# Kernel optimization log

Measured on AMD Instinct MI355X. Metric: run time of the kernel, lower is better.

## Reference

```python
import jax, jax.numpy as jnp
import numpy as np

B, L, IN_LEN = 1, 1024, 512
D_MODEL, N_LAYERS = 1024, 4
D_INNER = 2 * D_MODEL
D_STATE = 16
DT_RANK = D_MODEL // 16  # 64
D_CONV = 4
EPS = 1e-5


def setup_inputs() -> dict:
    key = jax.random.key(0)
    ks = jax.random.split(key, 12)
    s = 0.02
    # dt bias init as in mamba_ssm: softplus^{-1}(dt) with dt ~ logUniform(1e-3, 1e-1)
    dt = jnp.exp(jax.random.uniform(ks[7], (N_LAYERS, D_INNER)) * (jnp.log(0.1) - jnp.log(0.001)) + jnp.log(0.001))
    dt_bias = dt + jnp.log(-jnp.expm1(-dt))
    A_log = jnp.log(jnp.broadcast_to(jnp.arange(1, D_STATE + 1, dtype=jnp.float32), (N_LAYERS, D_INNER, D_STATE)))
    return {
        "input": jax.random.normal(ks[0], (B, L, IN_LEN), jnp.float32),
        "inference_parameters": 0,
        "input_w": jax.random.normal(ks[1], (D_MODEL, IN_LEN), jnp.float32) * s,
        "norm_w": jnp.ones((N_LAYERS, D_MODEL), jnp.float32),
        "norm_b": jnp.zeros((N_LAYERS, D_MODEL), jnp.float32),
        "in_proj_w": jax.random.normal(ks[2], (N_LAYERS, 2 * D_INNER, D_MODEL), jnp.float32) * s,
        "conv_w": jax.random.normal(ks[3], (N_LAYERS, D_INNER, D_CONV), jnp.float32) * 0.3,
        "conv_b": jnp.zeros((N_LAYERS, D_INNER), jnp.float32),
        "x_proj_w": jax.random.normal(ks[4], (N_LAYERS, DT_RANK + 2 * D_STATE, D_INNER), jnp.float32) * s,
        "dt_proj_w": jax.random.normal(ks[5], (N_LAYERS, D_INNER, DT_RANK), jnp.float32) * (DT_RANK ** -0.5),
        "dt_proj_b": dt_bias,
        "A_log": A_log,
        "ssm_D": jnp.ones((N_LAYERS, D_INNER), jnp.float32),
        "out_proj_w": jax.random.normal(ks[6], (N_LAYERS, D_MODEL, D_INNER), jnp.float32) * s,
    }


def _layer_norm(x, w, b):
    mu = x.mean(-1, keepdims=True)
    xc = x - mu
    var = (xc * xc).mean(-1, keepdims=True)
    return xc * jax.lax.rsqrt(var + EPS) * w + b


def _mamba(h, ipw, cw, cb, xpw, dtw, dtb, a_log, d_skip, opw):
    # h: [B, L, D_MODEL]
    seqlen = h.shape[1]
    xz = jnp.einsum('bld,ed->ble', h, ipw)  # [B, L, 2*D_INNER]
    x, z = jnp.split(xz, 2, axis=-1)
    # causal depthwise conv1d (kernel D_CONV, left pad D_CONV-1)
    xp = jnp.pad(x, ((0, 0), (D_CONV - 1, 0), (0, 0)))
    x = sum(cw[:, k] * xp[:, k:k + seqlen, :] for k in range(D_CONV)) + cb
    x = jax.nn.silu(x)
    x_dbl = jnp.einsum('bld,ed->ble', x, xpw)  # [B, L, DT_RANK + 2*D_STATE]
    dt = x_dbl[..., :DT_RANK]
    Bc = x_dbl[..., DT_RANK:DT_RANK + D_STATE]  # [B, L, D_STATE]
    Cc = x_dbl[..., DT_RANK + D_STATE:]          # [B, L, D_STATE]
    delta = jax.nn.softplus(jnp.einsum('blr,dr->bld', dt, dtw) + dtb)  # [B, L, D_INNER]
    A = -jnp.exp(a_log)                          # [D_INNER, D_STATE]
    dA = jnp.exp(delta[..., None] * A)           # [B, L, D_INNER, D_STATE]
    dBu = delta[..., None] * Bc[:, :, None, :] * x[..., None]

    def step(hc, t):
        dA_t, dBu_t, C_t = t
        hc = dA_t * hc + dBu_t                   # [B, D_INNER, D_STATE]
        return hc, jnp.einsum('bds,bs->bd', hc, C_t)

    h0 = jnp.zeros((x.shape[0], D_INNER, D_STATE), x.dtype)
    _, ys = jax.lax.scan(step, h0, (dA.transpose(1, 0, 2, 3), dBu.transpose(1, 0, 2, 3), Cc.transpose(1, 0, 2)))
    y = ys.transpose(1, 0, 2) + x * d_skip       # [B, L, D_INNER]
    y = y * jax.nn.silu(z)
    return jnp.einsum('bld,ed->ble', y, opw)     # [B, L, D_MODEL]


def reference(input, inference_parameters, input_w, norm_w, norm_b, in_proj_w, conv_w, conv_b, x_proj_w, dt_proj_w, dt_proj_b, A_log, ssm_D, out_proj_w):
    h = jnp.einsum('bli,di->bld', input, input_w)  # input_layer (no bias)
    res = None
    for i in range(N_LAYERS):
        res = h if res is None else h + res
        hn = _layer_norm(res, norm_w[i], norm_b[i])
        h = _mamba(hn, in_proj_w[i], conv_w[i], conv_b[i], x_proj_w[i], dt_proj_w[i], dt_proj_b[i], A_log[i], ssm_D[i], out_proj_w[i])
    # NOTE: the source forward returns hidden_states directly (norm_f is never applied)
    return h
```

## Files before the change

kernel.cpp:

```cpp
#include <hip/hip_runtime.h>
#include <hip/hip_bf16.h>
#include <math.h>

#define L_SEQ   1024
#define DMODEL  1024
#define DINNER  2048
#define DSTATE  16
#define DTRANK  64
#define NXP     96
#define LN_EPS  1e-5f
#define CHUNK   32
#define NCHUNK  (L_SEQ / CHUNK)
#define SK(l)   ((l) + ((l) >> 5))

typedef __bf16 bf16x8 __attribute__((ext_vector_type(8)));
typedef float  f32x4  __attribute__((ext_vector_type(4)));

__global__ __launch_bounds__(256)
void gemm_bt_bf16(const __hip_bfloat16* __restrict__ A,
                  const __hip_bfloat16* __restrict__ W,
                  float* __restrict__ C,
                  int K, int lda, int ldb, int ldc) {
    __shared__ __hip_bfloat16 As[128][32];
    __shared__ __hip_bfloat16 Bs[128][32];
    const int tid  = threadIdx.x;
    const int lane = tid & 63;
    const int wave = tid >> 6;
    const int m0 = blockIdx.y * 128, n0 = blockIdx.x * 128;
    const int wm = (wave >> 1) * 64, wn = (wave & 1) * 64;
    const int srow = tid >> 2, skcol = (tid & 3) << 3;
    const int fm = lane & 15, fk = (lane >> 4) << 3;

    f32x4 acc[4][4] = {};

    const __hip_bfloat16* Ap0 = A + (size_t)(m0 + srow) * lda + skcol;
    const __hip_bfloat16* Ap1 = Ap0 + (size_t)64 * lda;
    const __hip_bfloat16* Wp0 = W + (size_t)(n0 + srow) * ldb + skcol;
    const __hip_bfloat16* Wp1 = Wp0 + (size_t)64 * ldb;

    for (int k0 = 0; k0 < K; k0 += 32) {
        __syncthreads();
        __builtin_amdgcn_global_load_lds(
            (const __attribute__((address_space(1))) unsigned int*)(Ap0 + k0),
            (__attribute__((address_space(3))) unsigned int*)&As[srow][skcol], 16, 0, 0);
        __builtin_amdgcn_global_load_lds(
            (const __attribute__((address_space(1))) unsigned int*)(Ap1 + k0),
            (__attribute__((address_space(3))) unsigned int*)&As[64 + srow][skcol], 16, 0, 0);
        __builtin_amdgcn_global_load_lds(
            (const __attribute__((address_space(1))) unsigned int*)(Wp0 + k0),
            (__attribute__((address_space(3))) unsigned int*)&Bs[srow][skcol], 16, 0, 0);
        __builtin_amdgcn_global_load_lds(
            (const __attribute__((address_space(1))) unsigned int*)(Wp1 + k0),
            (__attribute__((address_space(3))) unsigned int*)&Bs[64 + srow][skcol], 16, 0, 0);
        __syncthreads();

        bf16x8 af[4], bfr[4];
        #pragma unroll
        for (int i = 0; i < 4; ++i) {
            af[i]  = *(const bf16x8*)&As[wm + i * 16 + fm][fk];
            bfr[i] = *(const bf16x8*)&Bs[wn + i * 16 + fm][fk];
        }
        #pragma unroll
        for (int mt = 0; mt < 4; ++mt)
            #pragma unroll
            for (int nt = 0; nt < 4; ++nt)
                acc[mt][nt] = __builtin_amdgcn_mfma_f32_16x16x32_bf16(
                    af[mt], bfr[nt], acc[mt][nt], 0, 0, 0);
    }

    const int crow = (lane >> 4) << 2;
    const int ccol = lane & 15;
    #pragma unroll
    for (int mt = 0; mt < 4; ++mt)
        #pragma unroll
        for (int nt = 0; nt < 4; ++nt) {
            float* cp = C + (size_t)(m0 + wm + mt * 16 + crow) * ldc
                          + n0 + wn + nt * 16 + ccol;
            #pragma unroll
            for (int r = 0; r < 4; ++r) cp[(size_t)r * ldc] = acc[mt][nt][r];
        }
}

__global__ __launch_bounds__(256)
void gemm_nt(const float* __restrict__ A, const float* __restrict__ W,
             float* __restrict__ C, int M, int N, int K,
             int lda, int ldb, int ldc) {
    __shared__ float As[16][64];
    __shared__ float Bs[16][64];
    const int tid = threadIdx.x;
    const int tx = tid & 15, ty = tid >> 4;
    const int m0 = blockIdx.y * 64, n0 = blockIdx.x * 64;
    const int lr = tid >> 2;
    const int lk = (tid & 3) << 2;
    float acc[4][4] = {};

    for (int k0 = 0; k0 < K; k0 += 16) {
        float4 av = make_float4(0.f, 0.f, 0.f, 0.f);
        float4 bv = make_float4(0.f, 0.f, 0.f, 0.f);
        const int am = m0 + lr;
        if (am < M) av = *(const float4*)(A + (size_t)am * lda + k0 + lk);
        const int bn = n0 + lr;
        if (bn < N) bv = *(const float4*)(W + (size_t)bn * ldb + k0 + lk);
        __syncthreads();
        As[lk + 0][lr] = av.x; As[lk + 1][lr] = av.y;
        As[lk + 2][lr] = av.z; As[lk + 3][lr] = av.w;
        Bs[lk + 0][lr] = bv.x; Bs[lk + 1][lr] = bv.y;
        Bs[lk + 2][lr] = bv.z; Bs[lk + 3][lr] = bv.w;
        __syncthreads();
        #pragma unroll
        for (int k = 0; k < 16; ++k) {
            const float4 a = *(const float4*)&As[k][ty << 2];
            const float4 b = *(const float4*)&Bs[k][tx << 2];
            acc[0][0] += a.x * b.x; acc[0][1] += a.x * b.y;
            acc[0][2] += a.x * b.z; acc[0][3] += a.x * b.w;
            acc[1][0] += a.y * b.x; acc[1][1] += a.y * b.y;
            acc[1][2] += a.y * b.z; acc[1][3] += a.y * b.w;
            acc[2][0] += a.z * b.x; acc[2][1] += a.z * b.y;
            acc[2][2] += a.z * b.z; acc[2][3] += a.z * b.w;
            acc[3][0] += a.w * b.x; acc[3][1] += a.w * b.y;
            acc[3][2] += a.w * b.z; acc[3][3] += a.w * b.w;
        }
    }
    #pragma unroll
    for (int i = 0; i < 4; ++i) {
        const int m = m0 + (ty << 2) + i;
        if (m < M) {
            #pragma unroll
            for (int j = 0; j < 4; ++j) {
                const int n = n0 + (tx << 2) + j;
                if (n < N) C[(size_t)m * ldc + n] = acc[i][j];
            }
        }
    }
}

__global__ __launch_bounds__(256)
void gemm_nn_softplus(const float* __restrict__ A, const float* __restrict__ B,
                      const float* __restrict__ bias, float* __restrict__ C,
                      int K, int lda, int ldb, int ldc) {
    __shared__ float As[16][64];
    __shared__ float Bs[16][64];
    const int t = threadIdx.x;
    const int tx = t & 15, ty = t >> 4;
    const int m0 = blockIdx.y * 64, n0 = blockIdx.x * 64;
    const int ar = t >> 2, ak = (t & 3) << 2;
    const int bk = t >> 4, bn = (t & 15) << 2;
    float acc[4][4] = {};

    for (int k0 = 0; k0 < K; k0 += 16) {
        const float4 av = *(const float4*)(A + (size_t)(m0 + ar) * lda + k0 + ak);
        const float4 bv = *(const float4*)(B + (size_t)(k0 + bk) * ldb + n0 + bn);
        __syncthreads();
        As[ak + 0][ar] = av.x; As[ak + 1][ar] = av.y;
        As[ak + 2][ar] = av.z; As[ak + 3][ar] = av.w;
        *(float4*)&Bs[bk][bn] = bv;
        __syncthreads();
        #pragma unroll
        for (int k = 0; k < 16; ++k) {
            const float4 a = *(const float4*)&As[k][ty << 2];
            const float4 b = *(const float4*)&Bs[k][tx << 2];
            acc[0][0] += a.x * b.x; acc[0][1] += a.x * b.y;
            acc[0][2] += a.x * b.z; acc[0][3] += a.x * b.w;
            acc[1][0] += a.y * b.x; acc[1][1] += a.y * b.y;
            acc[1][2] += a.y * b.z; acc[1][3] += a.y * b.w;
            acc[2][0] += a.z * b.x; acc[2][1] += a.z * b.y;
            acc[2][2] += a.z * b.z; acc[2][3] += a.z * b.w;
            acc[3][0] += a.w * b.x; acc[3][1] += a.w * b.y;
            acc[3][2] += a.w * b.z; acc[3][3] += a.w * b.w;
        }
    }
    #pragma unroll
    for (int i = 0; i < 4; ++i) {
        const int m = m0 + (ty << 2) + i;
        const float bb = bias[m];
        #pragma unroll
        for (int j = 0; j < 4; ++j) {
            const int n = n0 + (tx << 2) + j;
            const float v = acc[i][j] + bb;
            C[(size_t)m * ldc + n] = (v > 20.f) ? v : log1pf(expf(v));
        }
    }
}

__global__ __launch_bounds__(256)
void gemm_nn_splitk(const float* __restrict__ A, const float* __restrict__ B,
                    float* __restrict__ C, int lda, int ldb, int ldc, int kchunk) {
    __shared__ float As[32][32];
    __shared__ float Bs[32][64];
    const int t = threadIdx.x;
    const int tx = t & 15, ty = t >> 4;
    const int m0 = blockIdx.y * 32, n0 = blockIdx.x * 64;
    const int k0s = blockIdx.z * kchunk;
    const int ar = t >> 3, ak = (t & 7) << 2;
    const int bk = t >> 4, bn = (t & 15) << 2;
    float acc[2][4] = {};

    for (int k0 = k0s; k0 < k0s + kchunk; k0 += 32) {
        const float4 av = *(const float4*)(A + (size_t)(m0 + ar) * lda + k0 + ak);
        const float4 bv0 = *(const float4*)(B + (size_t)(k0 + bk) * ldb + n0 + bn);
        const float4 bv1 = *(const float4*)(B + (size_t)(k0 + bk + 16) * ldb + n0 + bn);
        __syncthreads();
        As[ak + 0][ar] = av.x; As[ak + 1][ar] = av.y;
        As[ak + 2][ar] = av.z; As[ak + 3][ar] = av.w;
        *(float4*)&Bs[bk][bn] = bv0;
        *(float4*)&Bs[bk + 16][bn] = bv1;
        __syncthreads();
        #pragma unroll
        for (int k = 0; k < 32; ++k) {
            const float a0 = As[k][(ty << 1) + 0];
            const float a1 = As[k][(ty << 1) + 1];
            const float4 b = *(const float4*)&Bs[k][tx << 2];
            acc[0][0] += a0 * b.x; acc[0][1] += a0 * b.y;
            acc[0][2] += a0 * b.z; acc[0][3] += a0 * b.w;
            acc[1][0] += a1 * b.x; acc[1][1] += a1 * b.y;
            acc[1][2] += a1 * b.z; acc[1][3] += a1 * b.w;
        }
    }
    #pragma unroll
    for (int i = 0; i < 2; ++i) {
        const int m = m0 + (ty << 1) + i;
        #pragma unroll
        for (int j = 0; j < 4; ++j)
            atomicAdd(&C[(size_t)m * ldc + n0 + (tx << 2) + j], acc[i][j]);
    }
}

__global__ __launch_bounds__(256)
void zero_f32(float* __restrict__ p, int n) {
    const int i = blockIdx.x * 256 + threadIdx.x;
    if (i < n) p[i] = 0.f;
}

__global__ __launch_bounds__(256)
void cast_f32_bf16(const float* __restrict__ in, __hip_bfloat16* __restrict__ out,
                   int n4) {
    const int i = blockIdx.x * 256 + threadIdx.x;
    if (i < n4) {
        const float4 v = *(const float4*)(in + (size_t)i * 4);
        __hip_bfloat16 h0 = __float2bfloat16(v.x), h1 = __float2bfloat16(v.y);
        __hip_bfloat16 h2 = __float2bfloat16(v.z), h3 = __float2bfloat16(v.w);
        ushort4 p;
        p.x = *(unsigned short*)&h0; p.y = *(unsigned short*)&h1;
        p.z = *(unsigned short*)&h2; p.w = *(unsigned short*)&h3;
        *(ushort4*)((unsigned short*)out + (size_t)i * 4) = p;
    }
}

__global__ __launch_bounds__(256)
void transpose_bc(const float* __restrict__ xdbl_T, float* __restrict__ xbc) {
    __shared__ float tile[32][33];
    const int t = threadIdx.x;
    const int l0 = blockIdx.x * 32;
    const int s = t >> 3, lc = (t & 7) << 2;
    const float4 v = *(const float4*)(xdbl_T + (size_t)(DTRANK + s) * L_SEQ + l0 + lc);
    tile[s][lc + 0] = v.x; tile[s][lc + 1] = v.y;
    tile[s][lc + 2] = v.z; tile[s][lc + 3] = v.w;
    __syncthreads();
    const int l = t >> 3, sc = (t & 7) << 2;
    float4 w;
    w.x = tile[sc + 0][l]; w.y = tile[sc + 1][l];
    w.z = tile[sc + 2][l]; w.w = tile[sc + 3][l];
    *(float4*)(xbc + (size_t)(l0 + l) * 32 + sc) = w;
}

__global__ __launch_bounds__(256)
void transpose_bf16(const unsigned short* __restrict__ in,
                    unsigned short* __restrict__ out, int R, int Cc) {
    __shared__ unsigned short tile[64][65];
    const int t = threadIdx.x;
    const int r0 = blockIdx.y * 64, c0 = blockIdx.x * 64;
    const int tr = t >> 3, tc8 = (t & 7) << 3;
    #pragma unroll
    for (int i = 0; i < 2; ++i) {
        const int r = tr + i * 32;
        const ushort4 v0 = *(const ushort4*)(in + (size_t)(r0 + r) * Cc + c0 + tc8);
        const ushort4 v1 = *(const ushort4*)(in + (size_t)(r0 + r) * Cc + c0 + tc8 + 4);
        tile[r][tc8 + 0] = v0.x; tile[r][tc8 + 1] = v0.y;
        tile[r][tc8 + 2] = v0.z; tile[r][tc8 + 3] = v0.w;
        tile[r][tc8 + 4] = v1.x; tile[r][tc8 + 5] = v1.y;
        tile[r][tc8 + 6] = v1.z; tile[r][tc8 + 7] = v1.w;
    }
    __syncthreads();
    #pragma unroll
    for (int i = 0; i < 2; ++i) {
        const int r = tr + i * 32;
        ushort4 w0, w1;
        w0.x = tile[tc8 + 0][r]; w0.y = tile[tc8 + 1][r];
        w0.z = tile[tc8 + 2][r]; w0.w = tile[tc8 + 3][r];
        w1.x = tile[tc8 + 4][r]; w1.y = tile[tc8 + 5][r];
        w1.z = tile[tc8 + 6][r]; w1.w = tile[tc8 + 7][r];
        *(ushort4*)(out + (size_t)(c0 + r) * R + r0 + tc8)     = w0;
        *(ushort4*)(out + (size_t)(c0 + r) * R + r0 + tc8 + 4) = w1;
    }
}

__global__ __launch_bounds__(256)
void add_ln(const float* __restrict__ h, float* __restrict__ res,
            __hip_bfloat16* __restrict__ hn, const float* __restrict__ w,
            const float* __restrict__ b, int is_first) {
    const int l = blockIdx.x;
    const int t = threadIdx.x;
    float v[4];
    float s = 0.f, ss = 0.f;
    #pragma unroll
    for (int j = 0; j < 4; ++j) {
        const int d = t + j * 256;
        float x = h[(size_t)l * DMODEL + d];
        if (!is_first) x += res[(size_t)l * DMODEL + d];
        res[(size_t)l * DMODEL + d] = x;
        v[j] = x; s += x; ss += x * x;
    }
    #pragma unroll
    for (int o = 32; o > 0; o >>= 1) {
        s  += __shfl_down(s, o);
        ss += __shfl_down(ss, o);
    }
    __shared__ float sm[4], sm2[4];
    const int wid = t >> 6;
    if ((t & 63) == 0) { sm[wid] = s; sm2[wid] = ss; }
    __syncthreads();
    s  = sm[0] + sm[1] + sm[2] + sm[3];
    ss = sm2[0] + sm2[1] + sm2[2] + sm2[3];
    const float mu  = s * (1.f / DMODEL);
    const float var = ss * (1.f / DMODEL) - mu * mu;
    const float r   = rsqrtf(var + LN_EPS);
    #pragma unroll
    for (int j = 0; j < 4; ++j) {
        const int d = t + j * 256;
        hn[(size_t)l * DMODEL + d] = __float2bfloat16((v[j] - mu) * r * w[d] + b[d]);
    }
}

__global__ __launch_bounds__(256)
void conv_silu_t(const float* __restrict__ xz_T, float* __restrict__ xc_T,
                 const float* __restrict__ cw, const float* __restrict__ cb) {
    const int d = blockIdx.x;
    const int t = threadIdx.x;
    __shared__ float row[L_SEQ];
    *(float4*)&row[t << 2] = *(const float4*)(xz_T + (size_t)d * L_SEQ + (t << 2));
    __syncthreads();
    const float w0 = cw[d * 4 + 0], w1 = cw[d * 4 + 1];
    const float w2 = cw[d * 4 + 2], w3 = cw[d * 4 + 3];
    const float bb = cb[d];
    float o[4];
    #pragma unroll
    for (int j = 0; j < 4; ++j) {
        const int l = (t << 2) + j;
        float acc = bb + w3 * row[l];
        if (l >= 1) acc += w2 * row[l - 1];
        if (l >= 2) acc += w1 * row[l - 2];
        if (l >= 3) acc += w0 * row[l - 3];
        const float sig = 1.f / (1.f + __expf(-acc));
        o[j] = acc * sig;
    }
    *(float4*)(xc_T + (size_t)d * L_SEQ + (t << 2)) = make_float4(o[0], o[1], o[2], o[3]);
}

__global__ __launch_bounds__(512)
void ssm_scan_t(const float* __restrict__ delta_T,
                const float* __restrict__ xc_T,
                const float* __restrict__ xbc,
                const float* __restrict__ xz_T,
                const float* __restrict__ alog,
                const float* __restrict__ dsk,
                __hip_bfloat16* __restrict__ y_T) {
    const int d = blockIdx.x;
    const int t = threadIdx.x;
    const int s = t & 15;
    const int c = t >> 4;

    __shared__ float sdl[L_SEQ + 32], sxl[L_SEQ + 32];
    __shared__ float sz[L_SEQ], sy[L_SEQ];
    __shared__ float saprod[NCHUNK][DSTATE];
    __shared__ float shloc[NCHUNK][DSTATE];
    __shared__ float shstart[NCHUNK][DSTATE];

    if (t < 256) {
        const float4 v = ((const float4*)(delta_T + (size_t)d * L_SEQ))[t];
        const int l = t << 2;
        sdl[SK(l)] = v.x; sdl[SK(l + 1)] = v.y;
        sdl[SK(l + 2)] = v.z; sdl[SK(l + 3)] = v.w;
        ((float4*)sz)[t] = ((const float4*)(xz_T + (size_t)(DINNER + d) * L_SEQ))[t];
    } else {
        const int tt = t - 256;
        const float4 v = ((const float4*)(xc_T + (size_t)d * L_SEQ))[tt];
        const int l = tt << 2;
        sxl[SK(l)] = v.x; sxl[SK(l + 1)] = v.y;
        sxl[SK(l + 2)] = v.z; sxl[SK(l + 3)] = v.w;
    }
    __syncthreads();

    const float A  = -expf(alog[d * DSTATE + s]);
    const int   l0 = c * CHUNK;

    float aprod = 1.f, h = 0.f;
    #pragma unroll 4
    for (int j = 0; j < CHUNK; ++j) {
        const int l = l0 + j;
        const float dl = sdl[SK(l)];
        const float da = __expf(dl * A);
        h = da * h + dl * xbc[(size_t)l * 32 + s] * sxl[SK(l)];
        aprod *= da;
    }
    saprod[c][s] = aprod;
    shloc[c][s]  = h;
    __syncthreads();

    if (c == 0) {
        float hs = 0.f;
        for (int cc = 0; cc < NCHUNK; ++cc) {
            shstart[cc][s] = hs;
            hs = saprod[cc][s] * hs + shloc[cc][s];
        }
    }
    __syncthreads();

    h = shstart[c][s];
    const float Dk = dsk[d];
    #pragma unroll 4
    for (int j = 0; j < CHUNK; ++j) {
        const int l = l0 + j;
        const float dl = sdl[SK(l)];
        const float xl = sxl[SK(l)];
        h = __expf(dl * A) * h + dl * xbc[(size_t)l * 32 + s] * xl;
        float cch = h * xbc[(size_t)l * 32 + 16 + s];
        cch += __shfl_xor(cch, 1, 16);
        cch += __shfl_xor(cch, 2, 16);
        cch += __shfl_xor(cch, 4, 16);
        cch += __shfl_xor(cch, 8, 16);
        if (s == 0) {
            const float zl  = sz[l];
            const float sig = 1.f / (1.f + __expf(-zl));
            sy[l] = (cch + xl * Dk) * (zl * sig);
        }
    }
    __syncthreads();

    if (t < 256) {
        const float4 v = ((const float4*)sy)[t];
        __hip_bfloat16 h0 = __float2bfloat16(v.x), h1 = __float2bfloat16(v.y);
        __hip_bfloat16 h2 = __float2bfloat16(v.z), h3 = __float2bfloat16(v.w);
        ushort4 p;
        p.x = *(unsigned short*)&h0; p.y = *(unsigned short*)&h1;
        p.z = *(unsigned short*)&h2; p.w = *(unsigned short*)&h3;
        *(ushort4*)((unsigned short*)y_T + (size_t)d * L_SEQ + (t << 2)) = p;
    }
}

extern "C" void kernel_launch(void* const* d_in, const int* in_sizes, int n_in,
                              void* d_out, int out_size, void* d_ws, size_t ws_size,
                              hipStream_t stream) {
    const float* input   = (const float*)d_in[0];
    const float* input_w = (const float*)d_in[2];
    const float* norm_w  = (const float*)d_in[3];
    const float* norm_b  = (const float*)d_in[4];
    const float* ipw     = (const float*)d_in[5];
    const float* cw      = (const float*)d_in[6];
    const float* cb      = (const float*)d_in[7];
    const float* xpw     = (const float*)d_in[8];
    const float* dtw     = (const float*)d_in[9];
    const float* dtb     = (const float*)d_in[10];
    const float* alog    = (const float*)d_in[11];
    const float* dsk     = (const float*)d_in[12];
    const float* opw     = (const float*)d_in[13];
    float* out = (float*)d_out;

    float* ws      = (float*)d_ws;
    float* h       = ws;
    float* res     = h       + (1u << 20);
    float* xz_T    = res     + (1u << 20);
    float* xc_T    = xz_T    + (4u << 20);
    float* xdbl_T  = xc_T    + (2u << 20);
    float* xbc     = xdbl_T  + (NXP * L_SEQ);
    float* delta_T = xbc     + (L_SEQ * 32);
    __hip_bfloat16* hn_bf  = (__hip_bfloat16*)(delta_T + (2u << 20));
    __hip_bfloat16* yT_bf  = hn_bf  + (1u << 20);
    __hip_bfloat16* y_bf   = yT_bf  + (2u << 20);
    __hip_bfloat16* ipw_bf = y_bf   + (2u << 20);
    __hip_bfloat16* opw_bf = ipw_bf + (4u << 20);

    const dim3 blk(256);

    gemm_nt<<<dim3(DMODEL / 64, L_SEQ / 64), blk, 0, stream>>>(
        input, input_w, h, L_SEQ, DMODEL, 512, 512, 512, DMODEL);

    for (int i = 0; i < 4; ++i) {
        cast_f32_bf16<<<(2 * DINNER * DMODEL / 4 + 255) / 256, blk, 0, stream>>>(
            ipw + (size_t)i * 2 * DINNER * DMODEL, ipw_bf, 2 * DINNER * DMODEL / 4);

        add_ln<<<L_SEQ, 256, 0, stream>>>(
            h, res, hn_bf, norm_w + i * DMODEL, norm_b + i * DMODEL, i == 0);

        gemm_bt_bf16<<<dim3(L_SEQ / 128, 2 * DINNER / 128), blk, 0, stream>>>(
            ipw_bf, hn_bf, xz_T, DMODEL, DMODEL, DMODEL, L_SEQ);

        conv_silu_t<<<DINNER, 256, 0, stream>>>(
            xz_T, xc_T, cw + i * DINNER * 4, cb + i * DINNER);

        zero_f32<<<(NXP * L_SEQ + 255) / 256, blk, 0, stream>>>(xdbl_T, NXP * L_SEQ);
        gemm_nn_splitk<<<dim3(L_SEQ / 64, 3, 8), blk, 0, stream>>>(
            xpw + (size_t)i * NXP * DINNER, xc_T, xdbl_T,
            DINNER, L_SEQ, L_SEQ, DINNER / 8);

        transpose_bc<<<L_SEQ / 32, 256, 0, stream>>>(xdbl_T, xbc);

        gemm_nn_softplus<<<dim3(L_SEQ / 64, DINNER / 64), blk, 0, stream>>>(
            dtw + (size_t)i * DINNER * DTRANK, xdbl_T, dtb + i * DINNER, delta_T,
            DTRANK, DTRANK, L_SEQ, L_SEQ);

        ssm_scan_t<<<DINNER, 512, 0, stream>>>(
            delta_T, xc_T, xbc, xz_T,
            alog + i * DINNER * DSTATE, dsk + i * DINNER, yT_bf);

        transpose_bf16<<<dim3(L_SEQ / 64, DINNER / 64), blk, 0, stream>>>(
            (const unsigned short*)yT_bf, (unsigned short*)y_bf, DINNER, L_SEQ);

        cast_f32_bf16<<<(DMODEL * DINNER / 4 + 255) / 256, blk, 0, stream>>>(
            opw + (size_t)i * DMODEL * DINNER, opw_bf, DMODEL * DINNER / 4);
        float* dst = (i == 3) ? out : h;
        gemm_bt_bf16<<<dim3(DMODEL / 128, L_SEQ / 128), blk, 0, stream>>>(
            y_bf, opw_bf, dst, DINNER, DINNER, DINNER, DMODEL);
    }
}
```

Measured before the change: 906.1 us.

## Halve scan chunk size, reuse chunk-local states, and split-K the out_proj GEMM

The SSM scan now uses 1024 threads with 16-step chunks. Each thread keeps its per-step cumulative decay and local state in registers, so the second pass becomes one fused multiply-add per step instead of recomputing the exponential recurrence. The out_proj GEMM, which launched only 64 blocks, is split four ways along K with atomicAdd into a zeroed output to fill more compute units. The costs are extra register pressure, a longer serial inter-chunk pass (64 chunks), an extra zeroing kernel, and atomic traffic with non-deterministic summation order.

```diff
diff --git a/kernel.cpp b/kernel.cpp
--- a/kernel.cpp
+++ b/kernel.cpp
@@ -9,7 +9,7 @@
 #define DTRANK  64
 #define NXP     96
 #define LN_EPS  1e-5f
-#define CHUNK   32
+#define CHUNK   16
 #define NCHUNK  (L_SEQ / CHUNK)
 #define SK(l)   ((l) + ((l) >> 5))
 
@@ -82,6 +82,73 @@
 }
 
 __global__ __launch_bounds__(256)
+void gemm_bt_bf16_sk(const __hip_bfloat16* __restrict__ A,
+                     const __hip_bfloat16* __restrict__ W,
+                     float* __restrict__ C,
+                     int kchunk, int lda, int ldb, int ldc) {
+    __shared__ __hip_bfloat16 As[128][32];
+    __shared__ __hip_bfloat16 Bs[128][32];
+    const int tid  = threadIdx.x;
+    const int lane = tid & 63;
+    const int wave = tid >> 6;
+    const int m0 = blockIdx.y * 128, n0 = blockIdx.x * 128;
+    const int k0s = blockIdx.z * kchunk;
+    const int wm = (wave >> 1) * 64, wn = (wave & 1) * 64;
+    const int srow = tid >> 2, skcol = (tid & 3) << 3;
+    const int fm = lane & 15, fk = (lane >> 4) << 3;
+
+    f32x4 acc[4][4] = {};
+
+    const __hip_bfloat16* Ap0 = A + (size_t)(m0 + srow) * lda + skcol;
+    const __hip_bfloat16* Ap1 = Ap0 + (size_t)64 * lda;
+    const __hip_bfloat16* Wp0 = W + (size_t)(n0 + srow) * ldb + skcol;
+    const __hip_bfloat16* Wp1 = Wp0 + (size_t)64 * ldb;
+
+    for (int k0 = k0s; k0 < k0s + kchunk; k0 += 32) {
+        __syncthreads();
+        __builtin_amdgcn_global_load_lds(
+            (const __attribute__((address_space(1))) unsigned int*)(Ap0 + k0),
+            (__attribute__((address_space(3))) unsigned int*)&As[srow][skcol], 16, 0, 0);
+        __builtin_amdgcn_global_load_lds(
+            (const __attribute__((address_space(1))) unsigned int*)(Ap1 + k0),
+            (__attribute__((address_space(3))) unsigned int*)&As[64 + srow][skcol], 16, 0, 0);
+        __builtin_amdgcn_global_load_lds(
+            (const __attribute__((address_space(1))) unsigned int*)(Wp0 + k0),
+            (__attribute__((address_space(3))) unsigned int*)&Bs[srow][skcol], 16, 0, 0);
+        __builtin_amdgcn_global_load_lds(
+            (const __attribute__((address_space(1))) unsigned int*)(Wp1 + k0),
+            (__attribute__((address_space(3))) unsigned int*)&Bs[64 + srow][skcol], 16, 0, 0);
+        __syncthreads();
+
+        bf16x8 af[4], bfr[4];
+        #pragma unroll
+        for (int i = 0; i < 4; ++i) {
+            af[i]  = *(const bf16x8*)&As[wm + i * 16 + fm][fk];
+            bfr[i] = *(const bf16x8*)&Bs[wn + i * 16 + fm][fk];
+        }
+        #pragma unroll
+        for (int mt = 0; mt < 4; ++mt)
+            #pragma unroll
+            for (int nt = 0; nt < 4; ++nt)
+                acc[mt][nt] = __builtin_amdgcn_mfma_f32_16x16x32_bf16(
+                    af[mt], bfr[nt], acc[mt][nt], 0, 0, 0);
+    }
+
+    const int crow = (lane >> 4) << 2;
+    const int ccol = lane & 15;
+    #pragma unroll
+    for (int mt = 0; mt < 4; ++mt)
+        #pragma unroll
+        for (int nt = 0; nt < 4; ++nt) {
+            float* cp = C + (size_t)(m0 + wm + mt * 16 + crow) * ldc
+                          + n0 + wn + nt * 16 + ccol;
+            #pragma unroll
+            for (int r = 0; r < 4; ++r)
+                atomicAdd(&cp[(size_t)r * ldc], acc[mt][nt][r]);
+        }
+}
+
+__global__ __launch_bounds__(256)
 void gemm_nt(const float* __restrict__ A, const float* __restrict__ W,
              float* __restrict__ C, int M, int N, int K,
              int lda, int ldb, int ldc) {
@@ -356,14 +423,14 @@
     *(float4*)(xc_T + (size_t)d * L_SEQ + (t << 2)) = make_float4(o[0], o[1], o[2], o[3]);
 }
 
-__global__ __launch_bounds__(512)
-void ssm_scan_t(const float* __restrict__ delta_T,
-                const float* __restrict__ xc_T,
-                const float* __restrict__ xbc,
-                const float* __restrict__ xz_T,
-                const float* __restrict__ alog,
-                const float* __restrict__ dsk,
-                __hip_bfloat16* __restrict__ y_T) {
+__global__ __launch_bounds__(1024)
+void ssm_scan_t2(const float* __restrict__ delta_T,
+                 const float* __restrict__ xc_T,
+                 const float* __restrict__ xbc,
+                 const float* __restrict__ xz_T,
+                 const float* __restrict__ alog,
+                 const float* __restrict__ dsk,
+                 __hip_bfloat16* __restrict__ y_T) {
     const int d = blockIdx.x;
     const int t = threadIdx.x;
     const int s = t & 15;
@@ -380,55 +447,58 @@
         const int l = t << 2;
         sdl[SK(l)] = v.x; sdl[SK(l + 1)] = v.y;
         sdl[SK(l + 2)] = v.z; sdl[SK(l + 3)] = v.w;
-        ((float4*)sz)[t] = ((const float4*)(xz_T + (size_t)(DINNER + d) * L_SEQ))[t];
-    } else {
+    } else if (t < 512) {
         const int tt = t - 256;
         const float4 v = ((const float4*)(xc_T + (size_t)d * L_SEQ))[tt];
         const int l = tt << 2;
         sxl[SK(l)] = v.x; sxl[SK(l + 1)] = v.y;
         sxl[SK(l + 2)] = v.z; sxl[SK(l + 3)] = v.w;
+    } else if (t < 768) {
+        ((float4*)sz)[t - 512] =
+            ((const float4*)(xz_T + (size_t)(DINNER + d) * L_SEQ))[t - 512];
     }
     __syncthreads();
 
     const float A  = -expf(alog[d * DSTATE + s]);
     const int   l0 = c * CHUNK;
 
+    float ap[CHUNK], hl[CHUNK];
     float aprod = 1.f, h = 0.f;
-    #pragma unroll 4
+    #pragma unroll
     for (int j = 0; j < CHUNK; ++j) {
         const int l = l0 + j;
         const float dl = sdl[SK(l)];
         const float da = __expf(dl * A);
         h = da * h + dl * xbc[(size_t)l * 32 + s] * sxl[SK(l)];
         aprod *= da;
+        ap[j] = aprod; hl[j] = h;
     }
     saprod[c][s] = aprod;
     shloc[c][s]  = h;
     __syncthreads();
 
-    if (c == 0) {
+    if (t < 16) {
         float hs = 0.f;
         for (int cc = 0; cc < NCHUNK; ++cc) {
-            shstart[cc][s] = hs;
-            hs = saprod[cc][s] * hs + shloc[cc][s];
-        }
-    }
-    __syncthreads();
-
-    h = shstart[c][s];
+            shstart[cc][t] = hs;
+            hs = saprod[cc][t] * hs + shloc[cc][t];
+        }
+    }
+    __syncthreads();
+
+    const float h0 = shstart[c][s];
     const float Dk = dsk[d];
-    #pragma unroll 4
+    #pragma unroll
     for (int j = 0; j < CHUNK; ++j) {
         const int l = l0 + j;
-        const float dl = sdl[SK(l)];
-        const float xl = sxl[SK(l)];
-        h = __expf(dl * A) * h + dl * xbc[(size_t)l * 32 + s] * xl;
-        float cch = h * xbc[(size_t)l * 32 + 16 + s];
+        const float hj = h0 * ap[j] + hl[j];
+        float cch = hj * xbc[(size_t)l * 32 + 16 + s];
         cch += __shfl_xor(cch, 1, 16);
         cch += __shfl_xor(cch, 2, 16);
         cch += __shfl_xor(cch, 4, 16);
         cch += __shfl_xor(cch, 8, 16);
         if (s == 0) {
+            const float xl  = sxl[SK(l)];
             const float zl  = sz[l];
             const float sig = 1.f / (1.f + __expf(-zl));
             sy[l] = (cch + xl * Dk) * (zl * sig);
@@ -438,11 +508,11 @@
 
     if (t < 256) {
         const float4 v = ((const float4*)sy)[t];
-        __hip_bfloat16 h0 = __float2bfloat16(v.x), h1 = __float2bfloat16(v.y);
-        __hip_bfloat16 h2 = __float2bfloat16(v.z), h3 = __float2bfloat16(v.w);
+        __hip_bfloat16 h0b = __float2bfloat16(v.x), h1b = __float2bfloat16(v.y);
+        __hip_bfloat16 h2b = __float2bfloat16(v.z), h3b = __float2bfloat16(v.w);
         ushort4 p;
-        p.x = *(unsigned short*)&h0; p.y = *(unsigned short*)&h1;
-        p.z = *(unsigned short*)&h2; p.w = *(unsigned short*)&h3;
+        p.x = *(unsigned short*)&h0b; p.y = *(unsigned short*)&h1b;
+        p.z = *(unsigned short*)&h2b; p.w = *(unsigned short*)&h3b;
         *(ushort4*)((unsigned short*)y_T + (size_t)d * L_SEQ + (t << 2)) = p;
     }
 }
@@ -508,7 +578,7 @@
             dtw + (size_t)i * DINNER * DTRANK, xdbl_T, dtb + i * DINNER, delta_T,
             DTRANK, DTRANK, L_SEQ, L_SEQ);
 
-        ssm_scan_t<<<DINNER, 512, 0, stream>>>(
+        ssm_scan_t2<<<DINNER, 1024, 0, stream>>>(
             delta_T, xc_T, xbc, xz_T,
             alog + i * DINNER * DSTATE, dsk + i * DINNER, yT_bf);
 
@@ -518,7 +588,8 @@
         cast_f32_bf16<<<(DMODEL * DINNER / 4 + 255) / 256, blk, 0, stream>>>(
             opw + (size_t)i * DMODEL * DINNER, opw_bf, DMODEL * DINNER / 4);
         float* dst = (i == 3) ? out : h;
-        gemm_bt_bf16<<<dim3(DMODEL / 128, L_SEQ / 128), blk, 0, stream>>>(
-            y_bf, opw_bf, dst, DINNER, DINNER, DINNER, DMODEL);
-    }
-}
+        zero_f32<<<(L_SEQ * DMODEL + 255) / 256, blk, 0, stream>>>(dst, L_SEQ * DMODEL);
+        gemm_bt_bf16_sk<<<dim3(DMODEL / 128, L_SEQ / 128, 4), blk, 0, stream>>>(
+            y_bf, opw_bf, dst, DINNER / 4, DINNER, DINNER, DMODEL);
+    }
+}
```

Result: no change. 913.2 us (+0.8%).
